# Performance work log

Hardware: AMD Instinct MI355X
Metric: run time of the kernel (lower is better)

The kernel has to match this reference:

```python
import jax, jax.numpy as jnp
import numpy as np


def setup_inputs() -> dict:
    key = jax.random.key(0)
    ks = jax.random.split(key, 9)
    B, T, D, H = 64, 512, 512, 512
    inp = {
        "x": jax.random.normal(ks[0], (B, T, D), dtype=jnp.float32),
        "W_c": jax.random.normal(ks[1], (D, H), dtype=jnp.float32) * 0.02,
        "W_i": jax.random.normal(ks[2], (D, H), dtype=jnp.float32) * 0.02,
        "W_f": jax.random.normal(ks[3], (D, H), dtype=jnp.float32) * 0.02,
        "W_o": jax.random.normal(ks[4], (D, H), dtype=jnp.float32) * 0.02,
        "U_c": jax.random.normal(ks[5], (H, H), dtype=jnp.float32) * 0.02,
        "U_i": jax.random.normal(ks[6], (H, H), dtype=jnp.float32) * 0.02,
        "U_f": jax.random.normal(ks[7], (H, H), dtype=jnp.float32) * 0.02,
        "U_o": jax.random.normal(ks[8], (H, H), dtype=jnp.float32) * 0.02,
        "b_c": jnp.zeros((H,), dtype=jnp.float32),
        "b_i": jnp.zeros((H,), dtype=jnp.float32),
        "b_f": jnp.zeros((H,), dtype=jnp.float32),
        "b_o": jnp.zeros((H,), dtype=jnp.float32),
    }
    return inp


def reference(x, W_c, W_i, W_f, W_o, U_c, U_i, U_f, U_o, b_c, b_i, b_f, b_o):
    # x: [B, T, D] -> scan over time-major [T, B, D]
    B, T, D = x.shape
    H = W_c.shape[1]
    h0 = jnp.zeros((B, H), dtype=x.dtype)
    c0 = jnp.zeros((B, H), dtype=x.dtype)

    # Precompute input projections for all timesteps (same math, hoisted
    # out of the recurrence since x does not depend on state).
    xt = jnp.transpose(x, (1, 0, 2))  # [T, B, D]
    xa = jnp.einsum('tbd,dh->tbh', xt, W_c) + b_c
    xi = jnp.einsum('tbd,dh->tbh', xt, W_i) + b_i
    xf = jnp.einsum('tbd,dh->tbh', xt, W_f) + b_f
    xo = jnp.einsum('tbd,dh->tbh', xt, W_o) + b_o

    def step(carry, elems):
        h, c = carry
        xa_t, xi_t, xf_t, xo_t = elems
        a = jnp.tanh(xa_t + h @ U_c)
        i = jax.nn.sigmoid(xi_t + h @ U_i)
        f = jax.nn.sigmoid(xf_t + h @ U_f)
        o = jax.nn.sigmoid(xo_t + h @ U_o)
        c_new = i * a + f * c
        h_new = o * jnp.tanh(c_new)
        return (h_new, c_new), h_new

    _, hs = jax.lax.scan(step, (h0, c0), (xa, xi, xf, xo))  # hs: [T, B, H]
    return jnp.transpose(hs, (1, 0, 2))  # return_sequence=True -> [B, T, H]
```

## Files before the change

### kernel.cpp

```cpp
#include <hip/hip_runtime.h>
#include <cstdint>
#include <cstddef>

typedef _Float16 half8  __attribute__((ext_vector_type(8)));
typedef float    floatx4 __attribute__((ext_vector_type(4)));
typedef unsigned long long ull;

#define B_  64
#define T_  512
#define D_  512
#define H_  512
#define NG  2048

static __device__ __forceinline__ float fast_sigmoid(float x) {
  return 1.0f / (1.0f + __expf(-x));
}
static __device__ __forceinline__ float fast_tanh(float x) {
  x = fminf(15.0f, fmaxf(-15.0f, x));
  float e = __expf(2.0f * x);
  return (e - 1.0f) / (e + 1.0f);
}

#define LDS_BARRIER() do {                                   \
    asm volatile("s_waitcnt lgkmcnt(0)" ::: "memory");       \
    __builtin_amdgcn_s_barrier();                            \
  } while (0)

#define TAGMASK 0x0000FFFF0000FFFFull

__global__ __launch_bounds__(256) void proj_kernel(
    const float* __restrict__ x,
    const float* __restrict__ Wc, const float* __restrict__ Wi,
    const float* __restrict__ Wf, const float* __restrict__ Wo,
    const float* __restrict__ bc, const float* __restrict__ bi,
    const float* __restrict__ bf2, const float* __restrict__ bo,
    _Float16* __restrict__ XG)
{
  const int tiles_n = NG / 64;
  int tM = blockIdx.x / tiles_n;
  int tN = blockIdx.x % tiles_n;
  int r0 = tM * 64;
  int t0 = r0 >> 6;
  int n0 = tN * 64;
  int g  = n0 >> 9;
  const float* W    = (g==0) ? Wc : (g==1) ? Wi : (g==2) ? Wf : Wo;
  const float* bias = (g==0) ? bc : (g==1) ? bi : (g==2) ? bf2 : bo;
  int j0 = n0 & (H_-1);

  __shared__ _Float16 Al[64*40];
  __shared__ _Float16 Bl[64*40];

  int tid  = threadIdx.x;
  int wave = tid >> 6;
  int lane = tid & 63;

  floatx4 acc[4] = {};

  int arow = tid >> 2;
  int ak0  = (tid & 3) * 8;
  const float* xsrc = x + ((size_t)arow * T_ + t0) * D_;

  int bcol = tid & 63;
  int bk0  = (tid >> 6) * 8;

  for (int k0 = 0; k0 < D_; k0 += 32) {
    half8 av;
    #pragma unroll
    for (int i = 0; i < 8; ++i) av[i] = (_Float16)xsrc[k0 + ak0 + i];
    *(half8*)&Al[arow*40 + ak0] = av;

    half8 bv;
    #pragma unroll
    for (int i = 0; i < 8; ++i)
      bv[i] = (_Float16)W[(size_t)(k0 + bk0 + i) * H_ + j0 + bcol];
    *(half8*)&Bl[bcol*40 + bk0] = bv;

    __syncthreads();

    half8 afrag = *(half8*)&Al[(wave*16 + (lane & 15))*40 + (lane >> 4)*8];
    #pragma unroll
    for (int ct = 0; ct < 4; ++ct) {
      half8 bfrag = *(half8*)&Bl[(ct*16 + (lane & 15))*40 + (lane >> 4)*8];
      acc[ct] = __builtin_amdgcn_mfma_f32_16x16x32_f16(afrag, bfrag, acc[ct], 0, 0, 0);
    }
    __syncthreads();
  }

  #pragma unroll
  for (int ct = 0; ct < 4; ++ct) {
    int col = n0 + ct*16 + (lane & 15);
    float bvs = bias[col & (H_-1)];
    #pragma unroll
    for (int i = 0; i < 4; ++i) {
      int row = r0 + wave*16 + (lane >> 4)*4 + i;
      XG[(size_t)row * NG + col] = (_Float16)(acc[ct][i] + bvs);
    }
  }
}

__global__ __launch_bounds__(256) void scan_kernel(
    const _Float16* __restrict__ XG,
    const float* __restrict__ Uc, const float* __restrict__ Ui,
    const float* __restrict__ Uf, const float* __restrict__ Uo,
    float* __restrict__ out, unsigned* __restrict__ dbuf)
{
  __shared__ _Float16 h_lds[16*640];

  int tid = threadIdx.x;
  int grp = blockIdx.x & 7;
  int member = blockIdx.x >> 3;

  int lane = tid & 63;
  int w    = tid >> 6;
  int c16  = lane & 15;
  int sub  = lane >> 4;
  int g    = c16 & 3;
  int jjl  = c16 >> 2;
  int jcol = member*16 + w*4 + jjl;
  int hi   = sub;
  bool pub = (g == 0) && (hi < 2);

  const float* Ug = (g==0) ? Uc : (g==1) ? Ui : (g==2) ? Uf : Uo;
  half8 uf[16];
  #pragma unroll
  for (int ks = 0; ks < 16; ++ks) {
    half8 v;
    #pragma unroll
    for (int q = 0; q < 8; ++q)
      v[q] = (_Float16)Ug[(size_t)(ks*32 + sub*8 + q) * H_ + jcol];
    uf[ks] = v;
  }

  int sm  = tid >> 3;
  int sb  = tid & 7;
  _Float16* stg = &h_lds[(sm >> 1)*640 + sb*40 + (sm & 1)*16];

  const _Float16* abase = &h_lds[c16*40 + sub*8];

  floatx4 c4 = {0.f, 0.f, 0.f, 0.f};
  float xg[4] = {0.f, 0.f, 0.f, 0.f};
  #pragma unroll
  for (int i = 0; i < 4; ++i)
    if (hi < 2)
      xg[i] = (float)XG[(size_t)(grp*8 + hi*4 + i) * NG + g*512 + jcol];

  for (int t = 0; t < T_; ++t) {
    LDS_BARRIER();

    {
      const ull* src8 = (const ull*)dbuf
          + ((size_t)(t & 1))*16384u + (size_t)grp*2048u + (size_t)tid*8u;
      ull want2 = (ull)(unsigned)(t & 0xFFFF) * 0x0000000100000001ull;
      ull w8[8];
      unsigned pend = 0xFFu;
      for (;;) {
        #pragma unroll
        for (int q = 0; q < 8; ++q)
          if (pend & (1u << q))
            w8[q] = __hip_atomic_load(src8 + q, __ATOMIC_RELAXED,
                                      __HIP_MEMORY_SCOPE_AGENT);
        unsigned npend = 0;
        #pragma unroll
        for (int q = 0; q < 8; ++q)
          if ((pend & (1u << q)) && ((w8[q] ^ want2) & TAGMASK))
            npend |= 1u << q;
        if (!npend) break;
        pend = npend;
        __builtin_amdgcn_s_sleep(2);
      }
      half8 hv0, hv1;
      #pragma unroll
      for (int q = 0; q < 4; ++q) {
        hv0[2*q]   = __builtin_bit_cast(_Float16, (unsigned short)((unsigned)w8[q]   >> 16));
        hv0[2*q+1] = __builtin_bit_cast(_Float16, (unsigned short)(w8[q]   >> 48));
        hv1[2*q]   = __builtin_bit_cast(_Float16, (unsigned short)((unsigned)w8[4+q] >> 16));
        hv1[2*q+1] = __builtin_bit_cast(_Float16, (unsigned short)(w8[4+q] >> 48));
      }
      *(half8*)stg       = hv0;
      *(half8*)(stg + 8) = hv1;
    }
    LDS_BARRIER();

    floatx4 a0 = {0.f,0.f,0.f,0.f}, a1 = {0.f,0.f,0.f,0.f};
    #pragma unroll
    for (int ks = 0; ks < 16; ks += 2) {
      half8 af0 = *(const half8*)(abase + ks*640);
      a0 = __builtin_amdgcn_mfma_f32_16x16x32_f16(af0, uf[ks],   a0, 0, 0, 0);
      half8 af1 = *(const half8*)(abase + (ks+1)*640);
      a1 = __builtin_amdgcn_mfma_f32_16x16x32_f16(af1, uf[ks+1], a1, 0, 0, 0);
    }

    float hval[4];
    #pragma unroll
    for (int i = 0; i < 4; ++i) {
      float pre = (a0[i] + a1[i]) + xg[i];
      float act = (g == 0) ? fast_tanh(pre) : fast_sigmoid(pre);
      float t1  = __shfl_xor(act, 1);
      float ia  = act * t1;
      float fv  = __shfl_xor(act, 2);
      float ov  = __shfl_xor(t1, 2);
      float cn  = fmaf(fv, c4[i], ia);
      c4[i] = cn;
      float hv = ov * fast_tanh(cn);
      hval[i] = hv;
      if (pub && (t + 1 < T_)) {
        unsigned wv = ((unsigned)__builtin_bit_cast(unsigned short,
                            (_Float16)hv) << 16)
                    | ((unsigned)(t + 1) & 0xFFFFu);
        unsigned widx = ((unsigned)((t + 1) & 1))*32768u + (unsigned)grp*4096u
                      + (unsigned)member*128u
                      + (unsigned)((hi*4 + i)*16 + w*4 + jjl);
        __hip_atomic_store(&dbuf[widx], wv,
                           __ATOMIC_RELAXED, __HIP_MEMORY_SCOPE_AGENT);
      }
    }

    if (pub) {
      #pragma unroll
      for (int i = 0; i < 4; ++i)
        out[((size_t)(grp*8 + hi*4 + i) * T_ + t) * H_ + jcol] = hval[i];
    }

    if (t + 1 < T_) {
      #pragma unroll
      for (int i = 0; i < 4; ++i)
        if (hi < 2)
          xg[i] = (float)XG[((size_t)(t + 1)*B_ + grp*8 + hi*4 + i) * NG
                            + g*512 + jcol];
    }
  }
}

extern "C" void kernel_launch(void* const* d_in, const int* in_sizes, int n_in,
                              void* d_out, int out_size, void* d_ws, size_t ws_size,
                              hipStream_t stream)
{
  const float* x  = (const float*)d_in[0];
  const float* Wc = (const float*)d_in[1];
  const float* Wi = (const float*)d_in[2];
  const float* Wf = (const float*)d_in[3];
  const float* Wo = (const float*)d_in[4];
  const float* Uc = (const float*)d_in[5];
  const float* Ui = (const float*)d_in[6];
  const float* Uf = (const float*)d_in[7];
  const float* Uo = (const float*)d_in[8];
  const float* bc = (const float*)d_in[9];
  const float* bi = (const float*)d_in[10];
  const float* bf2= (const float*)d_in[11];
  const float* bo = (const float*)d_in[12];
  float* out = (float*)d_out;

  const size_t XG_BYTES = (size_t)T_ * B_ * NG * sizeof(_Float16);
  const size_t DB_BYTES = (size_t)2 * 8 * 4096 * sizeof(unsigned);

  if (ws_size < XG_BYTES + DB_BYTES) return;

  _Float16* XG   = (_Float16*)d_ws;
  unsigned* dbuf = (unsigned*)((char*)d_ws + XG_BYTES);

  (void)hipMemsetAsync(dbuf, 0, DB_BYTES, stream);

  proj_kernel<<<dim3((T_*B_/64) * (NG/64)), dim3(256), 0, stream>>>(
      x, Wc, Wi, Wf, Wo, bc, bi, bf2, bo, XG);

  scan_kernel<<<dim3(256), dim3(256), 0, stream>>>(
      XG, Uc, Ui, Uf, Uo, out, dbuf);
}
```

Baseline: 2.065 ms.

## Fuse input projection into persistent scan kernel, dropping XG workspace

Removes the separate projection GEMM kernel and its half-precision XG intermediate. Each scan block now keeps W gate slices in registers, stages x rows for the next timestep in LDS and computes the input projection with MFMA inside the time loop, prefetching x two steps ahead. This avoids writing and rereading the large gate-preactivation buffer. The cost is extra registers and LDS per block and more MFMA work on the serial critical path of the recurrence.

Result: slower. 2.253 ms (+9.1%).

```diff
diff --git a/kernel.cpp b/kernel.cpp
--- a/kernel.cpp
+++ b/kernel.cpp
@@ -10,7 +10,6 @@
 #define T_  512
 #define D_  512
 #define H_  512
-#define NG  2048
 
 static __device__ __forceinline__ float fast_sigmoid(float x) {
   return 1.0f / (1.0f + __expf(-x));
@@ -28,83 +27,18 @@
 
 #define TAGMASK 0x0000FFFF0000FFFFull
 
-__global__ __launch_bounds__(256) void proj_kernel(
+__global__ __launch_bounds__(256) void scan_kernel(
     const float* __restrict__ x,
     const float* __restrict__ Wc, const float* __restrict__ Wi,
     const float* __restrict__ Wf, const float* __restrict__ Wo,
+    const float* __restrict__ Uc, const float* __restrict__ Ui,
+    const float* __restrict__ Uf, const float* __restrict__ Uo,
     const float* __restrict__ bc, const float* __restrict__ bi,
     const float* __restrict__ bf2, const float* __restrict__ bo,
-    _Float16* __restrict__ XG)
-{
-  const int tiles_n = NG / 64;
-  int tM = blockIdx.x / tiles_n;
-  int tN = blockIdx.x % tiles_n;
-  int r0 = tM * 64;
-  int t0 = r0 >> 6;
-  int n0 = tN * 64;
-  int g  = n0 >> 9;
-  const float* W    = (g==0) ? Wc : (g==1) ? Wi : (g==2) ? Wf : Wo;
-  const float* bias = (g==0) ? bc : (g==1) ? bi : (g==2) ? bf2 : bo;
-  int j0 = n0 & (H_-1);
-
-  __shared__ _Float16 Al[64*40];
-  __shared__ _Float16 Bl[64*40];
-
-  int tid  = threadIdx.x;
-  int wave = tid >> 6;
-  int lane = tid & 63;
-
-  floatx4 acc[4] = {};
-
-  int arow = tid >> 2;
-  int ak0  = (tid & 3) * 8;
-  const float* xsrc = x + ((size_t)arow * T_ + t0) * D_;
-
-  int bcol = tid & 63;
-  int bk0  = (tid >> 6) * 8;
-
-  for (int k0 = 0; k0 < D_; k0 += 32) {
-    half8 av;
-    #pragma unroll
-    for (int i = 0; i < 8; ++i) av[i] = (_Float16)xsrc[k0 + ak0 + i];
-    *(half8*)&Al[arow*40 + ak0] = av;
-
-    half8 bv;
-    #pragma unroll
-    for (int i = 0; i < 8; ++i)
-      bv[i] = (_Float16)W[(size_t)(k0 + bk0 + i) * H_ + j0 + bcol];
-    *(half8*)&Bl[bcol*40 + bk0] = bv;
-
-    __syncthreads();
-
-    half8 afrag = *(half8*)&Al[(wave*16 + (lane & 15))*40 + (lane >> 4)*8];
-    #pragma unroll
-    for (int ct = 0; ct < 4; ++ct) {
-      half8 bfrag = *(half8*)&Bl[(ct*16 + (lane & 15))*40 + (lane >> 4)*8];
-      acc[ct] = __builtin_amdgcn_mfma_f32_16x16x32_f16(afrag, bfrag, acc[ct], 0, 0, 0);
-    }
-    __syncthreads();
-  }
-
-  #pragma unroll
-  for (int ct = 0; ct < 4; ++ct) {
-    int col = n0 + ct*16 + (lane & 15);
-    float bvs = bias[col & (H_-1)];
-    #pragma unroll
-    for (int i = 0; i < 4; ++i) {
-      int row = r0 + wave*16 + (lane >> 4)*4 + i;
-      XG[(size_t)row * NG + col] = (_Float16)(acc[ct][i] + bvs);
-    }
-  }
-}
-
-__global__ __launch_bounds__(256) void scan_kernel(
-    const _Float16* __restrict__ XG,
-    const float* __restrict__ Uc, const float* __restrict__ Ui,
-    const float* __restrict__ Uf, const float* __restrict__ Uo,
     float* __restrict__ out, unsigned* __restrict__ dbuf)
 {
   __shared__ _Float16 h_lds[16*640];
+  __shared__ _Float16 xs_lds[16*640];
 
   int tid = threadIdx.x;
   int grp = blockIdx.x & 7;
@@ -120,15 +54,22 @@
   int hi   = sub;
   bool pub = (g == 0) && (hi < 2);
 
-  const float* Ug = (g==0) ? Uc : (g==1) ? Ui : (g==2) ? Uf : Uo;
-  half8 uf[16];
+  const float* Ug    = (g==0) ? Uc : (g==1) ? Ui : (g==2) ? Uf : Uo;
+  const float* Wg    = (g==0) ? Wc : (g==1) ? Wi : (g==2) ? Wf : Wo;
+  const float* biasg = (g==0) ? bc : (g==1) ? bi : (g==2) ? bf2 : bo;
+  float bvs = biasg[jcol];
+
+  half8 uf[16], wf[16];
   #pragma unroll
   for (int ks = 0; ks < 16; ++ks) {
-    half8 v;
-    #pragma unroll
-    for (int q = 0; q < 8; ++q)
-      v[q] = (_Float16)Ug[(size_t)(ks*32 + sub*8 + q) * H_ + jcol];
-    uf[ks] = v;
+    half8 vu, vw;
+    #pragma unroll
+    for (int q = 0; q < 8; ++q) {
+      vu[q] = (_Float16)Ug[(size_t)(ks*32 + sub*8 + q) * H_ + jcol];
+      vw[q] = (_Float16)Wg[(size_t)(ks*32 + sub*8 + q) * H_ + jcol];
+    }
+    uf[ks] = vu;
+    wf[ks] = vw;
   }
 
   int sm  = tid >> 3;
@@ -136,16 +77,56 @@
   _Float16* stg = &h_lds[(sm >> 1)*640 + sb*40 + (sm & 1)*16];
 
   const _Float16* abase = &h_lds[c16*40 + sub*8];
+  const _Float16* pbase = &xs_lds[c16*40 + sub*8];
+
+  int xr = tid >> 5;
+  int xc = tid & 31;
+  const float* xrow = x + (size_t)(grp*8 + xr) * T_ * D_ + (size_t)xc*16;
+  _Float16* xstg = &xs_lds[(xc >> 1)*640 + xr*40 + (xc & 1)*16];
+
+  float4 xr4[4];
+  #define LD_X(tt) do {                                                   \
+    const float4* p_ = (const float4*)(xrow + (size_t)(tt)*D_);           \
+    xr4[0] = p_[0]; xr4[1] = p_[1]; xr4[2] = p_[2]; xr4[3] = p_[3];       \
+  } while (0)
+  #define ST_X() do {                                                     \
+    half8 v0_, v1_;                                                       \
+    v0_[0]=(_Float16)xr4[0].x; v0_[1]=(_Float16)xr4[0].y;                 \
+    v0_[2]=(_Float16)xr4[0].z; v0_[3]=(_Float16)xr4[0].w;                 \
+    v0_[4]=(_Float16)xr4[1].x; v0_[5]=(_Float16)xr4[1].y;                 \
+    v0_[6]=(_Float16)xr4[1].z; v0_[7]=(_Float16)xr4[1].w;                 \
+    v1_[0]=(_Float16)xr4[2].x; v1_[1]=(_Float16)xr4[2].y;                 \
+    v1_[2]=(_Float16)xr4[2].z; v1_[3]=(_Float16)xr4[2].w;                 \
+    v1_[4]=(_Float16)xr4[3].x; v1_[5]=(_Float16)xr4[3].y;                 \
+    v1_[6]=(_Float16)xr4[3].z; v1_[7]=(_Float16)xr4[3].w;                 \
+    *(half8*)xstg       = v0_;                                            \
+    *(half8*)(xstg + 8) = v1_;                                            \
+  } while (0)
+
+  LD_X(0);
+  ST_X();
+  __syncthreads();
+  float xgc[4];
+  {
+    floatx4 p0 = {bvs, bvs, bvs, bvs}, p1 = {0.f, 0.f, 0.f, 0.f};
+    #pragma unroll
+    for (int ks = 0; ks < 16; ks += 2) {
+      half8 f0 = *(const half8*)(pbase + ks*640);
+      p0 = __builtin_amdgcn_mfma_f32_16x16x32_f16(f0, wf[ks],   p0, 0, 0, 0);
+      half8 f1 = *(const half8*)(pbase + (ks+1)*640);
+      p1 = __builtin_amdgcn_mfma_f32_16x16x32_f16(f1, wf[ks+1], p1, 0, 0, 0);
+    }
+    #pragma unroll
+    for (int i = 0; i < 4; ++i) xgc[i] = p0[i] + p1[i];
+  }
+  LD_X(1);
 
   floatx4 c4 = {0.f, 0.f, 0.f, 0.f};
-  float xg[4] = {0.f, 0.f, 0.f, 0.f};
-  #pragma unroll
-  for (int i = 0; i < 4; ++i)
-    if (hi < 2)
-      xg[i] = (float)XG[(size_t)(grp*8 + hi*4 + i) * NG + g*512 + jcol];
 
   for (int t = 0; t < T_; ++t) {
     LDS_BARRIER();
+
+    ST_X();
 
     {
       const ull* src8 = (const ull*)dbuf
@@ -193,7 +174,7 @@
     float hval[4];
     #pragma unroll
     for (int i = 0; i < 4; ++i) {
-      float pre = (a0[i] + a1[i]) + xg[i];
+      float pre = (a0[i] + a1[i]) + xgc[i];
       float act = (g == 0) ? fast_tanh(pre) : fast_sigmoid(pre);
       float t1  = __shfl_xor(act, 1);
       float ia  = act * t1;
@@ -221,12 +202,22 @@
         out[((size_t)(grp*8 + hi*4 + i) * T_ + t) * H_ + jcol] = hval[i];
     }
 
-    if (t + 1 < T_) {
-      #pragma unroll
-      for (int i = 0; i < 4; ++i)
-        if (hi < 2)
-          xg[i] = (float)XG[((size_t)(t + 1)*B_ + grp*8 + hi*4 + i) * NG
-                            + g*512 + jcol];
+    {
+      floatx4 p0 = {bvs, bvs, bvs, bvs}, p1 = {0.f, 0.f, 0.f, 0.f};
+      #pragma unroll
+      for (int ks = 0; ks < 16; ks += 2) {
+        half8 f0 = *(const half8*)(pbase + ks*640);
+        p0 = __builtin_amdgcn_mfma_f32_16x16x32_f16(f0, wf[ks],   p0, 0, 0, 0);
+        half8 f1 = *(const half8*)(pbase + (ks+1)*640);
+        p1 = __builtin_amdgcn_mfma_f32_16x16x32_f16(f1, wf[ks+1], p1, 0, 0, 0);
+      }
+      #pragma unroll
+      for (int i = 0; i < 4; ++i) xgc[i] = p0[i] + p1[i];
+    }
+
+    {
+      int xt = (t + 2 < T_) ? (t + 2) : (T_ - 1);
+      LD_X(xt);
     }
   }
 }
@@ -250,19 +241,14 @@
   const float* bo = (const float*)d_in[12];
   float* out = (float*)d_out;
 
-  const size_t XG_BYTES = (size_t)T_ * B_ * NG * sizeof(_Float16);
   const size_t DB_BYTES = (size_t)2 * 8 * 4096 * sizeof(unsigned);
 
-  if (ws_size < XG_BYTES + DB_BYTES) return;
-
-  _Float16* XG   = (_Float16*)d_ws;
-  unsigned* dbuf = (unsigned*)((char*)d_ws + XG_BYTES);
+  if (ws_size < DB_BYTES) return;
+
+  unsigned* dbuf = (unsigned*)d_ws;
 
   (void)hipMemsetAsync(dbuf, 0, DB_BYTES, stream);
 
-  proj_kernel<<<dim3((T_*B_/64) * (NG/64)), dim3(256), 0, stream>>>(
-      x, Wc, Wi, Wf, Wo, bc, bi, bf2, bo, XG);
-
   scan_kernel<<<dim3(256), dim3(256), 0, stream>>>(
-      XG, Uc, Ui, Uf, Uo, out, dbuf);
-}
+      x, Wc, Wi, Wf, Wo, Uc, Ui, Uf, Uo, bc, bi, bf2, bo, out, dbuf);
+}
```
